# Kernel tuning notes

Hardware: AMD Instinct MI355X
Metric: run time of the kernel (lower is better)

## Reference

```python
import jax, jax.numpy as jnp
import numpy as np
import math

B, N, K, H = 2, 2048, 1024, 16
S = K // H  # head dim = 64


def apply_rope(t):
    # t: [b, h, N, s] -> rotary position embedding (rotate-half convention)
    s = t.shape[-1]
    pos = jnp.arange(t.shape[2], dtype=jnp.float32)
    inv_freq = 1.0 / (10000.0 ** (jnp.arange(0, s, 2, dtype=jnp.float32) / s))
    ang = pos[:, None] * inv_freq[None, :]               # [N, s/2]
    cos = jnp.concatenate([jnp.cos(ang), jnp.cos(ang)], axis=-1)  # [N, s]
    sin = jnp.concatenate([jnp.sin(ang), jnp.sin(ang)], axis=-1)
    t1, t2 = t[..., : s // 2], t[..., s // 2:]
    rot = jnp.concatenate([-t2, t1], axis=-1)
    return t * cos + rot * sin


def setup_inputs() -> dict:
    key = jax.random.key(0)
    ks = jax.random.split(key, 6)
    sc = 1.0 / math.sqrt(K)
    x = jax.random.normal(ks[0], (B, N, K), dtype=jnp.float32)
    Wq = jax.random.normal(ks[1], (K, K), dtype=jnp.float32) * sc
    Wk = jax.random.normal(ks[2], (K, K), dtype=jnp.float32) * sc
    Wv = jax.random.normal(ks[3], (K, K), dtype=jnp.float32) * sc
    Wu = jax.random.normal(ks[4], (K, K), dtype=jnp.float32) * sc
    bu = jax.random.normal(ks[5], (K,), dtype=jnp.float32) * 0.01
    mask = jnp.tril(jnp.ones((N, N), dtype=jnp.int32))  # causal
    return {"x": x, "Wq": Wq, "Wk": Wk, "Wv": Wv, "Wu": Wu, "bu": bu, "mask": mask}


def reference(x, Wq, Wk, Wv, Wu, bu, mask):
    b, n, k = x.shape
    h, s = H, S
    # torch Linear: y = x @ W.T
    def proj(W):
        return (x @ W.T).reshape(b, n, h, s).transpose(0, 2, 1, 3)  # [b,h,n,s]
    Q = apply_rope(proj(Wq))
    Kh = apply_rope(proj(Wk))
    V = proj(Wv)
    scores = jnp.einsum('bhqs,bhks->bhqk', Q, Kh) / math.sqrt(s)
    scores = jnp.where(mask[None, None, :, :] == 0, -jnp.inf, scores)
    attn = jax.nn.softmax(scores, axis=-1)
    out = jnp.einsum('bhqk,bhks->bhqs', attn, V)           # [b,h,n,s]
    out = out.transpose(0, 2, 1, 3).reshape(b, n, k)
    return out @ Wu.T + bu
```

## Files before the change

### kernel.cpp

```cpp
#include <hip/hip_runtime.h>
#include <hip/hip_bf16.h>

#define Bq 2
#define Nq 2048
#define Kq 1024
#define Hq 16
#define Sq 64
#define Mq (Bq * Nq)

typedef __attribute__((ext_vector_type(4))) float f32x4;
typedef __attribute__((ext_vector_type(8))) short bf16x8;

__device__ unsigned short g_xb[(size_t)Mq * Kq];
__device__ unsigned short g_Wqb[Kq * Kq];
__device__ unsigned short g_Wkb[Kq * Kq];
__device__ unsigned short g_Wvb[Kq * Kq];
__device__ unsigned short g_Wub[Kq * Kq];
__device__ unsigned short g_Qb[(size_t)Bq * Hq * Nq * Sq];
__device__ unsigned short g_Kb[(size_t)Bq * Hq * Nq * Sq];
__device__ unsigned short g_Vb[(size_t)Bq * Hq * Nq * Sq];
__device__ unsigned short g_Vt[(size_t)Bq * Hq * Sq * Nq];
__device__ unsigned short g_Ao[(size_t)Mq * Kq];

__device__ __forceinline__ unsigned short f2bf(float f) {
    union { float f; unsigned int i; } u; u.f = f;
    unsigned int r = u.i + 0x7FFF + ((u.i >> 16) & 1);
    return (unsigned short)(r >> 16);
}
__device__ __forceinline__ float bf2f(unsigned short u) {
    union { unsigned int i; float f; } v; v.i = ((unsigned int)u) << 16;
    return v.f;
}
__device__ __forceinline__ void async16(const unsigned short* g, unsigned short* l) {
    __builtin_amdgcn_global_load_lds(
        (const __attribute__((address_space(1))) void*)g,
        (__attribute__((address_space(3))) void*)l, 16, 0, 0);
}

__global__ __launch_bounds__(256) void convert_all_kernel(
    const float* __restrict__ x,  const float* __restrict__ wq,
    const float* __restrict__ wk, const float* __restrict__ wv,
    const float* __restrict__ wu)
{
    int i = blockIdx.x * 256 + threadIdx.x;
    const float* src; unsigned short* dst; int off;
    if (i < 1048576) { src = x; dst = g_xb; off = i; }
    else {
        int j = i - 1048576;
        int which = j >> 18;
        off = j & 262143;
        src = (which == 0) ? wq : (which == 1) ? wk : (which == 2) ? wv : wu;
        dst = (which == 0) ? g_Wqb : (which == 1) ? g_Wkb : (which == 2) ? g_Wvb : g_Wub;
    }
    float4 v = ((const float4*)src)[off];
    ushort4 o;
    o.x = f2bf(v.x); o.y = f2bf(v.y); o.z = f2bf(v.z); o.w = f2bf(v.w);
    ((ushort4*)dst)[off] = o;
}

__global__ __launch_bounds__(256) void qkv_gemm_kernel()
{
    __shared__ __align__(16) unsigned short As[2][128][64];
    __shared__ __align__(16) unsigned short Bs[2][128][64];

    const int n0 = blockIdx.x * 128;
    const int m0 = blockIdx.y * 128;
    const int which = n0 >> 10;
    const unsigned short* A  = g_xb;
    const unsigned short* Bm = (which == 0) ? g_Wqb : (which == 1) ? g_Wkb : g_Wvb;
    unsigned short* dst      = (which == 0) ? g_Qb : (which == 1) ? g_Kb : g_Vb;
    const int nb = n0 & 1023;

    const int tid = threadIdx.x;
    const int w = tid >> 6, l = tid & 63;
    const int lane16 = l & 15, quad = l >> 4;
    const int wm = (w >> 1) * 64, wn = (w & 1) * 64;

    const int sr = l >> 3;
    const int sc = ((l & 7) ^ sr) * 8;
    const int rsw = (lane16 & 7);

    f32x4 acc[4][4];
#pragma unroll
    for (int mi = 0; mi < 4; ++mi)
#pragma unroll
        for (int ni = 0; ni < 4; ++ni) acc[mi][ni] = (f32x4){0.f, 0.f, 0.f, 0.f};

#pragma unroll
    for (int c = 0; c < 4; ++c) {
        async16(A  + (size_t)(m0 + 32 * w + 8 * c + sr) * Kq + sc, &As[0][32 * w + 8 * c][0]);
        async16(Bm + (size_t)(nb + 32 * w + 8 * c + sr) * Kq + sc, &Bs[0][32 * w + 8 * c][0]);
    }
    __syncthreads();

    int cur = 0;
    for (int kt = 0; kt < Kq; kt += 64) {
        if (kt + 64 < Kq) {
            int nxt = cur ^ 1;
#pragma unroll
            for (int c = 0; c < 4; ++c) {
                async16(A  + (size_t)(m0 + 32 * w + 8 * c + sr) * Kq + kt + 64 + sc, &As[nxt][32 * w + 8 * c][0]);
                async16(Bm + (size_t)(nb + 32 * w + 8 * c + sr) * Kq + kt + 64 + sc, &Bs[nxt][32 * w + 8 * c][0]);
            }
        }
#pragma unroll
        for (int ks = 0; ks < 2; ++ks) {
            bf16x8 af[4], bfr[4];
#pragma unroll
            for (int mi = 0; mi < 4; ++mi)
                af[mi]  = *(const bf16x8*)&As[cur][wm + mi * 16 + lane16][((ks * 4 + quad) ^ rsw) * 8];
#pragma unroll
            for (int ni = 0; ni < 4; ++ni)
                bfr[ni] = *(const bf16x8*)&Bs[cur][wn + ni * 16 + lane16][((ks * 4 + quad) ^ rsw) * 8];
#pragma unroll
            for (int mi = 0; mi < 4; ++mi)
#pragma unroll
                for (int ni = 0; ni < 4; ++ni)
                    acc[mi][ni] = __builtin_amdgcn_mfma_f32_16x16x32_bf16(af[mi], bfr[ni], acc[mi][ni], 0, 0, 0);
        }
        __syncthreads();
        cur ^= 1;
    }

#pragma unroll
    for (int mi = 0; mi < 4; ++mi)
#pragma unroll
        for (int ni = 0; ni < 4; ++ni)
#pragma unroll
            for (int r = 0; r < 4; ++r) {
                int m = m0 + wm + mi * 16 + quad * 4 + r;
                int n = n0 + wn + ni * 16 + lane16;
                unsigned short v = f2bf(acc[mi][ni][r]);
                int b = m >> 11, nn = m & 2047;
                int o = n & 1023, h = o >> 6, s = o & 63;
                dst[(((size_t)b * Hq + h) * Nq + nn) * Sq + s] = v;
            }
}

__global__ __launch_bounds__(256) void rope_vtrans_kernel()
{
    __shared__ unsigned short T[64][72];

    if (blockIdx.y < 2) {
        unsigned short* buf = (blockIdx.y == 0) ? g_Qb : g_Kb;
        const int idx = blockIdx.x * 256 + threadIdx.x;
        const int i  = idx & 31;
        const int n  = (idx >> 5) & (Nq - 1);
        const int bh = idx >> 16;
        const size_t base = ((size_t)bh * Nq + n) * Sq + i;

        float t1 = bf2f(buf[base]);
        float t2 = bf2f(buf[base + 32]);
        float inv_freq = exp2f((float)i * -0.41524101f);
        float ang = (float)n * inv_freq;
        float sn = __sinf(ang), cs = __cosf(ang);
        buf[base]      = f2bf(t1 * cs - t2 * sn);
        buf[base + 32] = f2bf(t2 * cs + t1 * sn);
    } else {
        if (blockIdx.x >= 1024) return;
        const int n0 = (blockIdx.x & 31) * 64;
        const int bh = blockIdx.x >> 5;
        const unsigned short* src = g_Vb + (size_t)bh * Nq * Sq;
        unsigned short* dst       = g_Vt + (size_t)bh * Sq * Nq;
        const int tid = threadIdx.x;
        const int r = tid >> 3, c8 = (tid & 7) * 8;

        uint4 a0 = *(const uint4*)(src + (size_t)(n0 + r) * Sq + c8);
        uint4 a1 = *(const uint4*)(src + (size_t)(n0 + r + 32) * Sq + c8);
        *(uint4*)&T[r][c8] = a0;
        *(uint4*)&T[r + 32][c8] = a1;
        __syncthreads();

        union { ushort4 u4[2]; unsigned short u[8]; } p0, p1;
#pragma unroll
        for (int j = 0; j < 8; ++j) { p0.u[j] = T[c8 + j][r]; p1.u[j] = T[c8 + j][r + 32]; }
        *(uint4*)(dst + (size_t)r * Nq + n0 + c8)        = *(uint4*)&p0;
        *(uint4*)(dst + (size_t)(r + 32) * Nq + n0 + c8) = *(uint4*)&p1;
    }
}

__global__ __launch_bounds__(256) void attn_kernel()
{
    const int bh = blockIdx.x;
    const int qt = 31 - (int)blockIdx.y;
    const int q0 = qt * 64;
    const unsigned short* Qp = g_Qb + (size_t)bh * Nq * Sq;
    const unsigned short* Kp = g_Kb + (size_t)bh * Nq * Sq;
    const unsigned short* Vp = g_Vt + (size_t)bh * Sq * Nq;

    __shared__ __align__(16) unsigned short Ks[2][64][64];
    __shared__ __align__(16) unsigned short Vs[2][64][64];
    __shared__ __align__(16) unsigned short On[16][72];
    __shared__ __align__(16) unsigned short Ps[64][72];

    const int tid = threadIdx.x;
    const int w = tid >> 6, l = tid & 63;
    const int lane16 = l & 15, quad = l >> 4;
    const int sr = l >> 3;
    const int sc = ((l & 7) ^ sr) * 8;
    const int rsw = (lane16 & 7);

    for (int i = tid; i < 16 * 72; i += 256)
        ((unsigned short*)On)[i] = (i < 64) ? 0x3F80 : 0;

    bf16x8 aq0 = *(const bf16x8*)(Qp + (size_t)(q0 + 16 * w + lane16) * Sq + quad * 8);
    bf16x8 aq1 = *(const bf16x8*)(Qp + (size_t)(q0 + 16 * w + lane16) * Sq + quad * 8 + 32);

    f32x4 Oacc[4];
    f32x4 Oext = (f32x4){0.f, 0.f, 0.f, 0.f};
#pragma unroll
    for (int ds = 0; ds < 4; ++ds) Oacc[ds] = (f32x4){0.f, 0.f, 0.f, 0.f};

    const float C1 = 0.18033688f;
    const float C2 = 11.54156036f;

    async16(Kp + (size_t)(16 * w + sr) * Sq + sc,     &Ks[0][16 * w][0]);
    async16(Kp + (size_t)(16 * w + 8 + sr) * Sq + sc, &Ks[0][16 * w + 8][0]);
    async16(Vp + (size_t)(16 * w + sr) * Nq + sc,     &Vs[0][16 * w][0]);
    async16(Vp + (size_t)(16 * w + 8 + sr) * Nq + sc, &Vs[0][16 * w + 8][0]);
    __syncthreads();

    int cur = 0;
    for (int kb = 0; kb <= qt; ++kb) {
        if (kb < qt) {
            int kn = (kb + 1) * 64;
            int nb2 = cur ^ 1;
            async16(Kp + (size_t)(kn + 16 * w + sr) * Sq + sc,     &Ks[nb2][16 * w][0]);
            async16(Kp + (size_t)(kn + 16 * w + 8 + sr) * Sq + sc, &Ks[nb2][16 * w + 8][0]);
            async16(Vp + (size_t)(16 * w + sr) * Nq + kn + sc,     &Vs[nb2][16 * w][0]);
            async16(Vp + (size_t)(16 * w + 8 + sr) * Nq + kn + sc, &Vs[nb2][16 * w + 8][0]);
        }

        f32x4 S[4];
#pragma unroll
        for (int kc = 0; kc < 4; ++kc) S[kc] = (f32x4){0.f, 0.f, 0.f, 0.f};
#pragma unroll
        for (int kc = 0; kc < 4; ++kc) {
            const unsigned short* krow = &Ks[cur][kc * 16 + lane16][0];
            bf16x8 bk0 = *(const bf16x8*)&krow[(quad ^ rsw) * 8];
            bf16x8 bk1 = *(const bf16x8*)&krow[((4 + quad) ^ rsw) * 8];
            S[kc] = __builtin_amdgcn_mfma_f32_16x16x32_bf16(aq0, bk0, S[kc], 0, 0, 0);
            S[kc] = __builtin_amdgcn_mfma_f32_16x16x32_bf16(aq1, bk1, S[kc], 0, 0, 0);
        }

        const int qbase = q0 + 16 * w + quad * 4;
        if (kb == qt) {
#pragma unroll
            for (int kc = 0; kc < 4; ++kc) {
                int kpos = kb * 64 + kc * 16 + lane16;
#pragma unroll
                for (int r = 0; r < 4; ++r)
                    S[kc][r] = (kpos <= qbase + r) ? exp2f(fmaf(S[kc][r], C1, -C2)) : 0.0f;
            }
        } else {
#pragma unroll
            for (int kc = 0; kc < 4; ++kc)
#pragma unroll
                for (int r = 0; r < 4; ++r)
                    S[kc][r] = exp2f(fmaf(S[kc][r], C1, -C2));
        }

#pragma unroll
        for (int kc = 0; kc < 4; ++kc)
#pragma unroll
            for (int r = 0; r < 4; ++r)
                Ps[16 * w + quad * 4 + r][kc * 16 + lane16] =
                    (unsigned short)(__float_as_uint(S[kc][r]) >> 16);

#pragma unroll
        for (int kk = 0; kk < 2; ++kk) {
            bf16x8 pa = *(const bf16x8*)&Ps[16 * w + lane16][kk * 32 + quad * 8];
            bf16x8 be = *(const bf16x8*)&On[lane16][kk * 32 + quad * 8];
#pragma unroll
            for (int ds = 0; ds < 4; ++ds) {
                bf16x8 vb = *(const bf16x8*)&Vs[cur][ds * 16 + lane16][((kk * 4 + quad) ^ rsw) * 8];
                Oacc[ds] = __builtin_amdgcn_mfma_f32_16x16x32_bf16(pa, vb, Oacc[ds], 0, 0, 0);
            }
            Oext = __builtin_amdgcn_mfma_f32_16x16x32_bf16(pa, be, Oext, 0, 0, 0);
        }

        __syncthreads();
        cur ^= 1;
    }

    const int b = bh >> 4, h = bh & 15;
    float inv[4];
#pragma unroll
    for (int r = 0; r < 4; ++r) {
        float lr = __shfl(Oext[r], quad * 16, 64);
        inv[r] = 1.0f / lr;
    }
#pragma unroll
    for (int ds = 0; ds < 4; ++ds)
#pragma unroll
        for (int r = 0; r < 4; ++r) {
            int nn = q0 + 16 * w + quad * 4 + r;
            g_Ao[((size_t)b * Nq + nn) * Kq + h * Sq + ds * 16 + lane16] =
                f2bf(Oacc[ds][r] * inv[r]);
        }
}

__global__ __launch_bounds__(256) void out_gemm_kernel(
    const float* __restrict__ bu, float* __restrict__ out)
{
    __shared__ __align__(16) unsigned short As[2][128][64];
    __shared__ __align__(16) unsigned short Bs[2][128][64];

    const int n0 = blockIdx.x * 128;
    const int m0 = blockIdx.y * 128;

    const int tid = threadIdx.x;
    const int w = tid >> 6, l = tid & 63;
    const int lane16 = l & 15, quad = l >> 4;
    const int wm = (w >> 1) * 64, wn = (w & 1) * 64;
    const int sr = l >> 3;
    const int sc = ((l & 7) ^ sr) * 8;
    const int rsw = (lane16 & 7);

    f32x4 acc[4][4];
#pragma unroll
    for (int mi = 0; mi < 4; ++mi)
#pragma unroll
        for (int ni = 0; ni < 4; ++ni) acc[mi][ni] = (f32x4){0.f, 0.f, 0.f, 0.f};

#pragma unroll
    for (int c = 0; c < 4; ++c) {
        async16(g_Ao  + (size_t)(m0 + 32 * w + 8 * c + sr) * Kq + sc, &As[0][32 * w + 8 * c][0]);
        async16(g_Wub + (size_t)(n0 + 32 * w + 8 * c + sr) * Kq + sc, &Bs[0][32 * w + 8 * c][0]);
    }
    __syncthreads();

    int cur = 0;
    for (int kt = 0; kt < Kq; kt += 64) {
        if (kt + 64 < Kq) {
            int nxt = cur ^ 1;
#pragma unroll
            for (int c = 0; c < 4; ++c) {
                async16(g_Ao  + (size_t)(m0 + 32 * w + 8 * c + sr) * Kq + kt + 64 + sc, &As[nxt][32 * w + 8 * c][0]);
                async16(g_Wub + (size_t)(n0 + 32 * w + 8 * c + sr) * Kq + kt + 64 + sc, &Bs[nxt][32 * w + 8 * c][0]);
            }
        }
#pragma unroll
        for (int ks = 0; ks < 2; ++ks) {
            bf16x8 af[4], bfr[4];
#pragma unroll
            for (int mi = 0; mi < 4; ++mi)
                af[mi]  = *(const bf16x8*)&As[cur][wm + mi * 16 + lane16][((ks * 4 + quad) ^ rsw) * 8];
#pragma unroll
            for (int ni = 0; ni < 4; ++ni)
                bfr[ni] = *(const bf16x8*)&Bs[cur][wn + ni * 16 + lane16][((ks * 4 + quad) ^ rsw) * 8];
#pragma unroll
            for (int mi = 0; mi < 4; ++mi)
#pragma unroll
                for (int ni = 0; ni < 4; ++ni)
                    acc[mi][ni] = __builtin_amdgcn_mfma_f32_16x16x32_bf16(af[mi], bfr[ni], acc[mi][ni], 0, 0, 0);
        }
        __syncthreads();
        cur ^= 1;
    }

#pragma unroll
    for (int mi = 0; mi < 4; ++mi)
#pragma unroll
        for (int ni = 0; ni < 4; ++ni)
#pragma unroll
            for (int r = 0; r < 4; ++r) {
                int m = m0 + wm + mi * 16 + quad * 4 + r;
                int n = n0 + wn + ni * 16 + lane16;
                out[(size_t)m * Kq + n] = acc[mi][ni][r] + bu[n];
            }
}

extern "C" void kernel_launch(void* const* d_in, const int* in_sizes, int n_in,
                              void* d_out, int out_size, void* d_ws, size_t ws_size,
                              hipStream_t stream)
{
    const float* x  = (const float*)d_in[0];
    const float* Wq = (const float*)d_in[1];
    const float* Wk = (const float*)d_in[2];
    const float* Wv = (const float*)d_in[3];
    const float* Wu = (const float*)d_in[4];
    const float* bu = (const float*)d_in[5];
    float* out = (float*)d_out;

    convert_all_kernel<<<8192, 256, 0, stream>>>(x, Wq, Wk, Wv, Wu);
    qkv_gemm_kernel<<<dim3(24, 32), 256, 0, stream>>>();
    rope_vtrans_kernel<<<dim3(8192, 3), 256, 0, stream>>>();
    attn_kernel<<<dim3(32, 32), 256, 0, stream>>>();
    out_gemm_kernel<<<dim3(8, 32), 256, 0, stream>>>(bu, out);
}
```

Before: 216.6 us.

## Enlarge attention query tile to 128 rows with 512-thread blocks

```diff
diff --git a/kernel.cpp b/kernel.cpp
--- a/kernel.cpp
+++ b/kernel.cpp
@@ -179,19 +179,20 @@
     }
 }
 
-__global__ __launch_bounds__(256) void attn_kernel()
+__global__ __launch_bounds__(512) void attn_kernel()
 {
     const int bh = blockIdx.x;
-    const int qt = 31 - (int)blockIdx.y;
-    const int q0 = qt * 64;
+    const int j  = blockIdx.y;
+    const int qt = (j < 8) ? (15 - j) : (j - 8);
+    const int q0 = qt * 128;
     const unsigned short* Qp = g_Qb + (size_t)bh * Nq * Sq;
     const unsigned short* Kp = g_Kb + (size_t)bh * Nq * Sq;
     const unsigned short* Vp = g_Vt + (size_t)bh * Sq * Nq;
 
     __shared__ __align__(16) unsigned short Ks[2][64][64];
     __shared__ __align__(16) unsigned short Vs[2][64][64];
-    __shared__ __align__(16) unsigned short On[16][72];
-    __shared__ __align__(16) unsigned short Ps[64][72];
+    __shared__ __align__(16) unsigned short Ps[128][64];
+    unsigned short* psf = &Ps[0][0];
 
     const int tid = threadIdx.x;
     const int w = tid >> 6, l = tid & 63;
@@ -200,11 +201,16 @@
     const int sc = ((l & 7) ^ sr) * 8;
     const int rsw = (lane16 & 7);
 
-    for (int i = tid; i < 16 * 72; i += 256)
-        ((unsigned short*)On)[i] = (i < 64) ? 0x3F80 : 0;
-
-    bf16x8 aq0 = *(const bf16x8*)(Qp + (size_t)(q0 + 16 * w + lane16) * Sq + quad * 8);
-    bf16x8 aq1 = *(const bf16x8*)(Qp + (size_t)(q0 + 16 * w + lane16) * Sq + quad * 8 + 32);
+    bf16x8 be;
+    {
+        short o = (lane16 == 0) ? (short)0x3F80 : (short)0;
+#pragma unroll
+        for (int i = 0; i < 8; ++i) be[i] = o;
+    }
+
+    const int qlo = q0 + 16 * w;
+    bf16x8 aq0 = *(const bf16x8*)(Qp + (size_t)(qlo + lane16) * Sq + quad * 8);
+    bf16x8 aq1 = *(const bf16x8*)(Qp + (size_t)(qlo + lane16) * Sq + quad * 8 + 32);
 
     f32x4 Oacc[4];
     f32x4 Oext = (f32x4){0.f, 0.f, 0.f, 0.f};
@@ -214,69 +220,71 @@
     const float C1 = 0.18033688f;
     const float C2 = 11.54156036f;
 
-    async16(Kp + (size_t)(16 * w + sr) * Sq + sc,     &Ks[0][16 * w][0]);
-    async16(Kp + (size_t)(16 * w + 8 + sr) * Sq + sc, &Ks[0][16 * w + 8][0]);
-    async16(Vp + (size_t)(16 * w + sr) * Nq + sc,     &Vs[0][16 * w][0]);
-    async16(Vp + (size_t)(16 * w + 8 + sr) * Nq + sc, &Vs[0][16 * w + 8][0]);
+    async16(Kp + (size_t)(8 * w + sr) * Sq + sc, &Ks[0][8 * w][0]);
+    async16(Vp + (size_t)(8 * w + sr) * Nq + sc, &Vs[0][8 * w][0]);
     __syncthreads();
 
+    const int ntiles = 2 * qt + 2;
     int cur = 0;
-    for (int kb = 0; kb <= qt; ++kb) {
-        if (kb < qt) {
+    for (int kb = 0; kb < ntiles; ++kb) {
+        if (kb + 1 < ntiles) {
             int kn = (kb + 1) * 64;
             int nb2 = cur ^ 1;
-            async16(Kp + (size_t)(kn + 16 * w + sr) * Sq + sc,     &Ks[nb2][16 * w][0]);
-            async16(Kp + (size_t)(kn + 16 * w + 8 + sr) * Sq + sc, &Ks[nb2][16 * w + 8][0]);
-            async16(Vp + (size_t)(16 * w + sr) * Nq + kn + sc,     &Vs[nb2][16 * w][0]);
-            async16(Vp + (size_t)(16 * w + 8 + sr) * Nq + kn + sc, &Vs[nb2][16 * w + 8][0]);
-        }
-
-        f32x4 S[4];
-#pragma unroll
-        for (int kc = 0; kc < 4; ++kc) S[kc] = (f32x4){0.f, 0.f, 0.f, 0.f};
-#pragma unroll
-        for (int kc = 0; kc < 4; ++kc) {
-            const unsigned short* krow = &Ks[cur][kc * 16 + lane16][0];
-            bf16x8 bk0 = *(const bf16x8*)&krow[(quad ^ rsw) * 8];
-            bf16x8 bk1 = *(const bf16x8*)&krow[((4 + quad) ^ rsw) * 8];
-            S[kc] = __builtin_amdgcn_mfma_f32_16x16x32_bf16(aq0, bk0, S[kc], 0, 0, 0);
-            S[kc] = __builtin_amdgcn_mfma_f32_16x16x32_bf16(aq1, bk1, S[kc], 0, 0, 0);
-        }
-
-        const int qbase = q0 + 16 * w + quad * 4;
-        if (kb == qt) {
+            async16(Kp + (size_t)(kn + 8 * w + sr) * Sq + sc, &Ks[nb2][8 * w][0]);
+            async16(Vp + (size_t)(8 * w + sr) * Nq + kn + sc, &Vs[nb2][8 * w][0]);
+        }
+
+        if (kb * 64 <= qlo + 15) {
+            f32x4 S[4];
+#pragma unroll
+            for (int kc = 0; kc < 4; ++kc) S[kc] = (f32x4){0.f, 0.f, 0.f, 0.f};
 #pragma unroll
             for (int kc = 0; kc < 4; ++kc) {
-                int kpos = kb * 64 + kc * 16 + lane16;
-#pragma unroll
-                for (int r = 0; r < 4; ++r)
-                    S[kc][r] = (kpos <= qbase + r) ? exp2f(fmaf(S[kc][r], C1, -C2)) : 0.0f;
-            }
-        } else {
+                const unsigned short* krow = &Ks[cur][kc * 16 + lane16][0];
+                bf16x8 bk0 = *(const bf16x8*)&krow[(quad ^ rsw) * 8];
+                bf16x8 bk1 = *(const bf16x8*)&krow[((4 + quad) ^ rsw) * 8];
+                S[kc] = __builtin_amdgcn_mfma_f32_16x16x32_bf16(aq0, bk0, S[kc], 0, 0, 0);
+                S[kc] = __builtin_amdgcn_mfma_f32_16x16x32_bf16(aq1, bk1, S[kc], 0, 0, 0);
+            }
+
+            const int qbase = qlo + quad * 4;
+            if (kb * 64 + 63 > qlo) {
+#pragma unroll
+                for (int kc = 0; kc < 4; ++kc) {
+                    int kpos = kb * 64 + kc * 16 + lane16;
+#pragma unroll
+                    for (int r = 0; r < 4; ++r)
+                        S[kc][r] = (kpos <= qbase + r) ? exp2f(fmaf(S[kc][r], C1, -C2)) : 0.0f;
+                }
+            } else {
+#pragma unroll
+                for (int kc = 0; kc < 4; ++kc)
+#pragma unroll
+                    for (int r = 0; r < 4; ++r)
+                        S[kc][r] = exp2f(fmaf(S[kc][r], C1, -C2));
+            }
+
 #pragma unroll
             for (int kc = 0; kc < 4; ++kc)
 #pragma unroll
-                for (int r = 0; r < 4; ++r)
-                    S[kc][r] = exp2f(fmaf(S[kc][r], C1, -C2));
-        }
-
-#pragma unroll
-        for (int kc = 0; kc < 4; ++kc)
-#pragma unroll
-            for (int r = 0; r < 4; ++r)
-                Ps[16 * w + quad * 4 + r][kc * 16 + lane16] =
-                    (unsigned short)(__float_as_uint(S[kc][r]) >> 16);
-
-#pragma unroll
-        for (int kk = 0; kk < 2; ++kk) {
-            bf16x8 pa = *(const bf16x8*)&Ps[16 * w + lane16][kk * 32 + quad * 8];
-            bf16x8 be = *(const bf16x8*)&On[lane16][kk * 32 + quad * 8];
-#pragma unroll
-            for (int ds = 0; ds < 4; ++ds) {
-                bf16x8 vb = *(const bf16x8*)&Vs[cur][ds * 16 + lane16][((kk * 4 + quad) ^ rsw) * 8];
-                Oacc[ds] = __builtin_amdgcn_mfma_f32_16x16x32_bf16(pa, vb, Oacc[ds], 0, 0, 0);
-            }
-            Oext = __builtin_amdgcn_mfma_f32_16x16x32_bf16(pa, be, Oext, 0, 0, 0);
+                for (int r = 0; r < 4; ++r) {
+                    int prow = 16 * w + quad * 4 + r;
+                    psf[(prow * 64 + kc * 16 + lane16) ^ ((prow & 7) << 3)] =
+                        (unsigned short)(__float_as_uint(S[kc][r]) >> 16);
+                }
+
+            const int prow2 = 16 * w + lane16;
+#pragma unroll
+            for (int kk = 0; kk < 2; ++kk) {
+                bf16x8 pa = *(const bf16x8*)(psf +
+                    ((prow2 * 64 + kk * 32 + quad * 8) ^ (rsw << 3)));
+#pragma unroll
+                for (int ds = 0; ds < 4; ++ds) {
+                    bf16x8 vb = *(const bf16x8*)&Vs[cur][ds * 16 + lane16][((kk * 4 + quad) ^ rsw) * 8];
+                    Oacc[ds] = __builtin_amdgcn_mfma_f32_16x16x32_bf16(pa, vb, Oacc[ds], 0, 0, 0);
+                }
+                Oext = __builtin_amdgcn_mfma_f32_16x16x32_bf16(pa, be, Oext, 0, 0, 0);
+            }
         }
 
         __syncthreads();
@@ -294,7 +302,7 @@
     for (int ds = 0; ds < 4; ++ds)
 #pragma unroll
         for (int r = 0; r < 4; ++r) {
-            int nn = q0 + 16 * w + quad * 4 + r;
+            int nn = qlo + quad * 4 + r;
             g_Ao[((size_t)b * Nq + nn) * Kq + h * Sq + ds * 16 + lane16] =
                 f2bf(Oacc[ds][r] * inv[r]);
         }
@@ -386,6 +394,6 @@
     convert_all_kernel<<<8192, 256, 0, stream>>>(x, Wq, Wk, Wv, Wu);
     qkv_gemm_kernel<<<dim3(24, 32), 256, 0, stream>>>();
     rope_vtrans_kernel<<<dim3(8192, 3), 256, 0, stream>>>();
-    attn_kernel<<<dim3(32, 32), 256, 0, stream>>>();
+    attn_kernel<<<dim3(32, 16), 512, 0, stream>>>();
     out_gemm_kernel<<<dim3(8, 32), 256, 0, stream>>>(bu, out);
 }
```

Result: no change. 219.3 us (+1.2%).
